# Optimization experiments

Measured on AMD Instinct MI355X. Metric: run time of the kernel, lower is better.

The kernel has to match this reference:

```python
import jax, jax.numpy as jnp
import numpy as np

DIM = 768
NUM_HEADS = 12
HEAD_DIM = DIM // NUM_HEADS
GRID = 32  # H == W
EPS = 1e-6


def setup_inputs() -> dict:
    key = jax.random.key(0)
    ks = jax.random.split(key, 8)
    B, N = 8, GRID * GRID
    x = jax.random.normal(ks[0], (B, N, DIM), dtype=jnp.float32)
    policy = jax.random.randint(ks[1], (B, N, 1), 0, 2).astype(jnp.float32)
    qkv_w = jax.random.normal(ks[2], (3 * DIM, DIM), dtype=jnp.float32) * 0.02
    qkv_b = jax.random.normal(ks[3], (3 * DIM,), dtype=jnp.float32) * 0.02
    proj_w = jax.random.normal(ks[4], (DIM, DIM), dtype=jnp.float32) * 0.02
    proj_b = jax.random.normal(ks[5], (DIM,), dtype=jnp.float32) * 0.02
    rel_pos_h = jax.random.normal(ks[6], (2 * GRID - 1, HEAD_DIM), dtype=jnp.float32) * 0.02
    rel_pos_w = jax.random.normal(ks[7], (2 * GRID - 1, HEAD_DIM), dtype=jnp.float32) * 0.02
    return {"x": x, "policy": policy, "qkv_w": qkv_w, "qkv_b": qkv_b,
            "proj_w": proj_w, "proj_b": proj_b,
            "rel_pos_h": rel_pos_h, "rel_pos_w": rel_pos_w, "H": GRID, "W": GRID}


def _attention(x, policy, qkv_w, qkv_b, proj_w, proj_b, rel_pos_h, rel_pos_w, H, W):
    B, N, C = x.shape
    nh, hd = NUM_HEADS, C // NUM_HEADS
    scale = hd ** (-0.5)
    # qkv projection: [B,N,3C] -> [3, B*nh, N, hd]
    qkv = (x @ qkv_w.T + qkv_b).reshape(B, N, 3, nh, hd)
    qkv = qkv.transpose(2, 0, 3, 1, 4).reshape(3, B * nh, N, hd)
    q, k, v = qkv[0], qkv[1], qkv[2]
    attn = jnp.einsum("bqd,bkd->bqk", q * scale, k)  # [B*nh, N, N]
    # decomposed relative position bias (q_size == k_size == (H, W))
    coords = jnp.arange(H)
    Rh = rel_pos_h[coords[:, None] - coords[None, :] + (H - 1)]  # [H,H,hd]
    coords_w = jnp.arange(W)
    Rw = rel_pos_w[coords_w[:, None] - coords_w[None, :] + (W - 1)]  # [W,W,hd]
    r_q = q.reshape(B * nh, H, W, hd)
    rel_h = jnp.einsum("bhwc,hkc->bhwk", r_q, Rh)  # [B*nh,H,W,H]
    rel_w = jnp.einsum("bhwc,wkc->bhwk", r_q, Rw)  # [B*nh,H,W,W]
    attn = (attn.reshape(B * nh, H, W, H, W)
            + rel_h[:, :, :, :, None]
            + rel_w[:, :, :, None, :]).reshape(B * nh, N, N)
    # policy-masked softmax
    attn = attn.reshape(B, nh, N, N)
    ap = policy.reshape(B, 1, 1, N)
    ap = ap + (1.0 - ap) * jnp.eye(N, dtype=ap.dtype)  # always attend to self
    max_att = jnp.max(attn, axis=-1, keepdims=True)
    e = jnp.exp(attn - max_att).astype(jnp.float32) * ap.astype(jnp.float32)
    attn = ((e + EPS / N) / (jnp.sum(e, axis=-1, keepdims=True) + EPS)).astype(x.dtype)
    out = jnp.einsum("bqk,bkd->bqd", attn.reshape(B * nh, N, N), v)
    out = out.reshape(B, nh, N, hd).transpose(0, 2, 1, 3).reshape(B, N, C)
    return out @ proj_w.T + proj_b


def reference(x, policy, qkv_w, qkv_b, proj_w, proj_b, rel_pos_h, rel_pos_w, H, W):
    return _attention(x, policy, qkv_w, qkv_b, proj_w, proj_b, rel_pos_h, rel_pos_w, H, W)
```

## Files before the change

kernel.cpp:

```cpp
#include <hip/hip_runtime.h>
#include <hip/hip_bf16.h>

#define B_   8
#define N_   1024
#define C_   768
#define NH_  12
#define HD_  64
#define BH_  96
#define EPS_ 1e-6f
#define EPSN_ (1e-6f / 1024.0f)

typedef __bf16 bf16;
typedef __attribute__((ext_vector_type(8))) __bf16  bf16x8;
typedef __attribute__((ext_vector_type(4))) __bf16  bf16x4;
typedef __attribute__((ext_vector_type(4))) float   floatx4;

#define MFMA16(a, b, c) __builtin_amdgcn_mfma_f32_16x16x32_bf16((a), (b), (c), 0, 0, 0)

__global__ __launch_bounds__(256) void f2b_kernel(const float* __restrict__ in,
                                                  bf16* __restrict__ out, int n4) {
  int i = blockIdx.x * 256 + threadIdx.x;
  if (i < n4) {
    float4 v = ((const float4*)in)[i];
    bf16x4 o = {(bf16)v.x, (bf16)v.y, (bf16)v.z, (bf16)v.w};
    ((bf16x4*)out)[i] = o;
  }
}

__global__ __launch_bounds__(256) void rel_kernel(const float* __restrict__ in,
                                                  bf16* __restrict__ out) {
  int i = blockIdx.x * 256 + threadIdx.x;
  int r = i >> 6;
  out[i] = (r < 63) ? (bf16)in[i] : (bf16)0.0f;
}

__global__ __launch_bounds__(256) void gemm_qkv(
    const bf16* __restrict__ X, const bf16* __restrict__ W,
    const float* __restrict__ bias,
    bf16* __restrict__ Qb, bf16* __restrict__ Kb, bf16* __restrict__ Vb) {
  __shared__ bf16 As[128][72];
  __shared__ bf16 Bs[128][72];
  const int tid = threadIdx.x;
  const int wid = tid >> 6, lane = tid & 63, quad = lane >> 4, c16 = lane & 15;
  const int wm = (wid >> 1) * 64, wn = (wid & 1) * 64;
  const int m0 = blockIdx.x * 128, n0 = blockIdx.y * 128;
  floatx4 acc[4][4];
#pragma unroll
  for (int i = 0; i < 4; ++i)
#pragma unroll
    for (int j = 0; j < 4; ++j) acc[i][j] = {0.f, 0.f, 0.f, 0.f};

  for (int k0 = 0; k0 < 768; k0 += 64) {
    __syncthreads();
#pragma unroll
    for (int t = 0; t < 4; ++t) {
      int task = t * 256 + tid;
      int r = task >> 3, c8 = (task & 7) * 8;
      *(bf16x8*)&As[r][c8] = *(const bf16x8*)(X + (size_t)(m0 + r) * 768 + k0 + c8);
      *(bf16x8*)&Bs[r][c8] = *(const bf16x8*)(W + (size_t)(n0 + r) * 768 + k0 + c8);
    }
    __syncthreads();
#pragma unroll
    for (int kw = 0; kw < 2; ++kw) {
      bf16x8 af[4], bfr[4];
#pragma unroll
      for (int i = 0; i < 4; ++i) af[i] = *(bf16x8*)&As[wm + i * 16 + c16][kw * 32 + quad * 8];
#pragma unroll
      for (int j = 0; j < 4; ++j) bfr[j] = *(bf16x8*)&Bs[wn + j * 16 + c16][kw * 32 + quad * 8];
#pragma unroll
      for (int i = 0; i < 4; ++i)
#pragma unroll
        for (int j = 0; j < 4; ++j) acc[i][j] = MFMA16(af[i], bfr[j], acc[i][j]);
    }
  }
#pragma unroll
  for (int jt = 0; jt < 4; ++jt) {
    int j = n0 + wn + jt * 16 + c16;
    float bj = bias[j];
    int t = j / 768, rem = j - t * 768;
    int head = rem >> 6, d = rem & 63;
    bf16* base = (t == 0) ? Qb : (t == 1) ? Kb : Vb;
#pragma unroll
    for (int it = 0; it < 4; ++it)
#pragma unroll
      for (int reg = 0; reg < 4; ++reg) {
        int m = m0 + wm + it * 16 + quad * 4 + reg;
        int bb = m >> 10, n = m & 1023;
        float v = acc[it][jt][reg] + bj;
        size_t idx = (t == 2)
            ? (((size_t)bb * NH_ + head) * HD_ + d) * N_ + n
            : (((size_t)bb * NH_ + head) * N_ + n) * HD_ + d;
        base[idx] = (bf16)v;
      }
  }
}

__global__ __launch_bounds__(256) void vsum_kernel(const bf16* __restrict__ Vb,
                                                   float* __restrict__ Vsum) {
  const int bh = blockIdx.x;
  const int d = threadIdx.x >> 2, part = threadIdx.x & 3;
  const bf16* Vg = Vb + (size_t)bh * (N_ * HD_) + d * N_ + part * 256;
  float s = 0.f;
  for (int i = 0; i < 32; ++i) {
    bf16x8 v = *(const bf16x8*)(Vg + i * 8);
#pragma unroll
    for (int e = 0; e < 8; ++e) s += (float)v[e];
  }
  __shared__ float red[64][4];
  red[d][part] = s;
  __syncthreads();
  if (part == 0) Vsum[bh * 64 + d] = red[d][0] + red[d][1] + red[d][2] + red[d][3];
}

__global__ __launch_bounds__(256) void attn_mfma(
    const bf16* __restrict__ Qb, const bf16* __restrict__ Kb,
    const bf16* __restrict__ Vb, const float* __restrict__ policy,
    const bf16* __restrict__ Rh, const bf16* __restrict__ Rw,
    const float* __restrict__ Vsum, bf16* __restrict__ AO) {
  const int bh = blockIdx.x, qt = blockIdx.y;
  const int b = bh / NH_, head = bh % NH_;
  __shared__ __align__(16) char smem[46592];
  bf16 (*Qs)[72]  = (bf16(*)[72])(smem);
  bf16 (*Ks)[72]  = (bf16(*)[72])(smem + 9216);
  bf16 (*Vt)[72]  = (bf16(*)[72])(smem + 18432);
  float (*RHs)[33] = (float(*)[33])(smem + 27648);
  float (*RWs)[33] = (float(*)[33])(smem + 36096);
  bf16* pol = (bf16*)(smem + 44544);
  const int tid = threadIdx.x;
  const int wid = tid >> 6, lane = tid & 63, quad = lane >> 4, c16 = lane & 15;
  bf16 (*Ptw)[72] = (bf16(*)[72])(smem) + wid * 16;
  const floatx4 zero4 = {0.f, 0.f, 0.f, 0.f};

  const bf16* Qg = Qb + ((size_t)bh * N_ + qt * 64) * HD_;
  const bf16* Kg = Kb + (size_t)bh * (N_ * HD_);
  const bf16* Vg = Vb + (size_t)bh * (N_ * HD_);

#pragma unroll
  for (int t = 0; t < 2; ++t) {
    int task = t * 256 + tid;
    int r = task >> 3, c8 = (task & 7) * 8;
    *(bf16x8*)&Qs[r][c8] = *(const bf16x8*)(Qg + r * 64 + c8);
    *(bf16x8*)&Ks[r][c8] = *(const bf16x8*)(Rh + r * 64 + c8);
  }
  {
    float4 p = ((const float4*)(policy + (size_t)b * N_))[tid];
    bf16x4 pb = {(bf16)p.x, (bf16)p.y, (bf16)p.z, (bf16)p.w};
    *(bf16x4*)&pol[tid * 4] = pb;
  }
  __syncthreads();

  bf16x8 aq0 = *(bf16x8*)&Qs[wid * 16 + c16][quad * 8];
  bf16x8 aq1 = *(bf16x8*)&Qs[wid * 16 + c16][32 + quad * 8];

  {
    floatx4 racc[4];
#pragma unroll
    for (int nt = 0; nt < 4; ++nt) {
      bf16x8 b0 = *(bf16x8*)&Ks[nt * 16 + c16][quad * 8];
      bf16x8 b1 = *(bf16x8*)&Ks[nt * 16 + c16][32 + quad * 8];
      racc[nt] = MFMA16(aq1, b1, MFMA16(aq0, b0, zero4));
    }
#pragma unroll
    for (int nt = 0; nt < 4; ++nt)
#pragma unroll
      for (int reg = 0; reg < 4; ++reg) {
        int rloc = wid * 16 + quad * 4 + reg;
        int hh = 2 * qt + (rloc >> 5);
        int j = nt * 16 + c16;
        int krow = hh + 31 - j;
        if ((unsigned)krow < 32u) RHs[rloc][krow] = racc[nt][reg];
      }
  }
  __syncthreads();
#pragma unroll
  for (int t = 0; t < 2; ++t) {
    int task = t * 256 + tid;
    int r = task >> 3, c8 = (task & 7) * 8;
    *(bf16x8*)&Ks[r][c8] = *(const bf16x8*)(Rw + r * 64 + c8);
  }
  __syncthreads();
  {
    floatx4 racc[4];
#pragma unroll
    for (int nt = 0; nt < 4; ++nt) {
      bf16x8 b0 = *(bf16x8*)&Ks[nt * 16 + c16][quad * 8];
      bf16x8 b1 = *(bf16x8*)&Ks[nt * 16 + c16][32 + quad * 8];
      racc[nt] = MFMA16(aq1, b1, MFMA16(aq0, b0, zero4));
    }
#pragma unroll
    for (int nt = 0; nt < 4; ++nt)
#pragma unroll
      for (int reg = 0; reg < 4; ++reg) {
        int rloc = wid * 16 + quad * 4 + reg;
        int ww = rloc & 31;
        int j = nt * 16 + c16;
        int kcol = ww + 31 - j;
        if ((unsigned)kcol < 32u) RWs[rloc][kcol] = racc[nt][reg];
      }
  }

  float l_part[4] = {0.f, 0.f, 0.f, 0.f};
  floatx4 o_acc[4];
#pragma unroll
  for (int i = 0; i < 4; ++i) o_acc[i] = zero4;
  int nqr[4];
#pragma unroll
  for (int reg = 0; reg < 4; ++reg) nqr[reg] = qt * 64 + wid * 16 + quad * 4 + reg;

  for (int kt = 0; kt < 16; ++kt) {
    __syncthreads();
#pragma unroll
    for (int t = 0; t < 2; ++t) {
      int task = t * 256 + tid;
      int r = task >> 3, c8 = (task & 7) * 8;
      *(bf16x8*)&Ks[r][c8] = *(const bf16x8*)(Kg + (size_t)(kt * 64 + r) * 64 + c8);
      *(bf16x8*)&Vt[r][c8] = *(const bf16x8*)(Vg + (size_t)r * N_ + kt * 64 + c8);
    }
    __syncthreads();

    floatx4 s[4];
#pragma unroll
    for (int nt = 0; nt < 4; ++nt) {
      bf16x8 bk0 = *(bf16x8*)&Ks[nt * 16 + c16][quad * 8];
      bf16x8 bk1 = *(bf16x8*)&Ks[nt * 16 + c16][32 + quad * 8];
      s[nt] = MFMA16(aq1, bk1, MFMA16(aq0, bk0, zero4));
    }
    float pm[4];
#pragma unroll
    for (int nt = 0; nt < 4; ++nt) pm[nt] = (float)pol[kt * 64 + nt * 16 + c16];

#pragma unroll
    for (int reg = 0; reg < 4; ++reg) {
      const int rloc = wid * 16 + quad * 4 + reg;
      const int nq = nqr[reg];
      const float rh0 = RHs[rloc][kt * 2], rh1 = RHs[rloc][kt * 2 + 1];
#pragma unroll
      for (int nt = 0; nt < 4; ++nt) {
        float sv = s[nt][reg] * 0.125f + ((nt < 2) ? rh0 : rh1)
                 + RWs[rloc][(nt & 1) * 16 + c16];
        int kg = kt * 64 + nt * 16 + c16;
        float mask = (kg == nq) ? 1.f : pm[nt];
        float e = __expf(sv) * mask;
        l_part[reg] += e;
        Ptw[quad * 4 + reg][nt * 16 + c16] = (bf16)e;
      }
    }

#pragma unroll
    for (int kw2 = 0; kw2 < 2; ++kw2) {
      bf16x8 ap = *(bf16x8*)&Ptw[c16][kw2 * 32 + quad * 8];
#pragma unroll
      for (int dt = 0; dt < 4; ++dt) {
        bf16x8 bv = *(bf16x8*)&Vt[dt * 16 + c16][kw2 * 32 + quad * 8];
        o_acc[dt] = MFMA16(ap, bv, o_acc[dt]);
      }
    }
  }

  float inv[4];
#pragma unroll
  for (int reg = 0; reg < 4; ++reg) {
    float l = l_part[reg];
#pragma unroll
    for (int d = 1; d < 16; d <<= 1) l += __shfl_xor(l, d, 64);
    inv[reg] = 1.f / (l + EPS_);
  }
#pragma unroll
  for (int dt = 0; dt < 4; ++dt) {
    int d = dt * 16 + c16;
    float vs = Vsum[bh * 64 + d];
#pragma unroll
    for (int reg = 0; reg < 4; ++reg) {
      float o = (o_acc[dt][reg] + EPSN_ * vs) * inv[reg];
      AO[((size_t)b * N_ + nqr[reg]) * C_ + head * HD_ + d] = (bf16)o;
    }
  }
}

__global__ __launch_bounds__(256) void gemm_proj(
    const bf16* __restrict__ A, const bf16* __restrict__ W,
    const float* __restrict__ bias, float* __restrict__ Out) {
  __shared__ bf16 As[128][72];
  __shared__ bf16 Bs[128][72];
  const int tid = threadIdx.x;
  const int wid = tid >> 6, lane = tid & 63, quad = lane >> 4, c16 = lane & 15;
  const int wm = (wid >> 1) * 64, wn = (wid & 1) * 64;
  const int m0 = blockIdx.x * 128, n0 = blockIdx.y * 128;
  floatx4 acc[4][4];
#pragma unroll
  for (int i = 0; i < 4; ++i)
#pragma unroll
    for (int j = 0; j < 4; ++j) acc[i][j] = {0.f, 0.f, 0.f, 0.f};

  for (int k0 = 0; k0 < 768; k0 += 64) {
    __syncthreads();
#pragma unroll
    for (int t = 0; t < 4; ++t) {
      int task = t * 256 + tid;
      int r = task >> 3, c8 = (task & 7) * 8;
      *(bf16x8*)&As[r][c8] = *(const bf16x8*)(A + (size_t)(m0 + r) * 768 + k0 + c8);
      *(bf16x8*)&Bs[r][c8] = *(const bf16x8*)(W + (size_t)(n0 + r) * 768 + k0 + c8);
    }
    __syncthreads();
#pragma unroll
    for (int kw = 0; kw < 2; ++kw) {
      bf16x8 af[4], bfr[4];
#pragma unroll
      for (int i = 0; i < 4; ++i) af[i] = *(bf16x8*)&As[wm + i * 16 + c16][kw * 32 + quad * 8];
#pragma unroll
      for (int j = 0; j < 4; ++j) bfr[j] = *(bf16x8*)&Bs[wn + j * 16 + c16][kw * 32 + quad * 8];
#pragma unroll
      for (int i = 0; i < 4; ++i)
#pragma unroll
        for (int j = 0; j < 4; ++j) acc[i][j] = MFMA16(af[i], bfr[j], acc[i][j]);
    }
  }
#pragma unroll
  for (int jt = 0; jt < 4; ++jt) {
    int j = n0 + wn + jt * 16 + c16;
    float bj = bias[j];
#pragma unroll
    for (int it = 0; it < 4; ++it)
#pragma unroll
      for (int reg = 0; reg < 4; ++reg) {
        int m = m0 + wm + it * 16 + quad * 4 + reg;
        Out[(size_t)m * 768 + j] = acc[it][jt][reg] + bj;
      }
  }
}

extern "C" void kernel_launch(void* const* d_in, const int* in_sizes, int n_in,
                              void* d_out, int out_size, void* d_ws, size_t ws_size,
                              hipStream_t stream) {
  const float* x      = (const float*)d_in[0];
  const float* policy = (const float*)d_in[1];
  const float* qkv_w  = (const float*)d_in[2];
  const float* qkv_b  = (const float*)d_in[3];
  const float* proj_w = (const float*)d_in[4];
  const float* proj_b = (const float*)d_in[5];
  const float* relh   = (const float*)d_in[6];
  const float* relw   = (const float*)d_in[7];

  char* ws = (char*)d_ws;
  bf16* Xbf   = (bf16*)(ws);
  bf16* Wqkv  = (bf16*)(ws + 12582912);
  bf16* Wproj = (bf16*)(ws + 16121856);
  bf16* Rhb   = (bf16*)(ws + 17301504);
  bf16* Rwb   = (bf16*)(ws + 17309696);
  bf16* Qb    = (bf16*)(ws + 17317888);
  bf16* Kb    = (bf16*)(ws + 29900800);
  bf16* Vb    = (bf16*)(ws + 42483712);
  bf16* AOb   = (bf16*)(ws + 55066624);
  float* Vsum = (float*)(ws + 67649536);

  f2b_kernel<<<6144, 256, 0, stream>>>(x, Xbf, 1572864);
  f2b_kernel<<<1728, 256, 0, stream>>>(qkv_w, Wqkv, 442368);
  f2b_kernel<<<576, 256, 0, stream>>>(proj_w, Wproj, 147456);
  rel_kernel<<<16, 256, 0, stream>>>(relh, Rhb);
  rel_kernel<<<16, 256, 0, stream>>>(relw, Rwb);

  gemm_qkv<<<dim3(64, 18), 256, 0, stream>>>(Xbf, Wqkv, qkv_b, Qb, Kb, Vb);
  vsum_kernel<<<BH_, 256, 0, stream>>>(Vb, Vsum);
  attn_mfma<<<dim3(BH_, 16), 256, 0, stream>>>(Qb, Kb, Vb, policy, Rhb, Rwb,
                                               Vsum, AOb);
  gemm_proj<<<dim3(64, 6), 256, 0, stream>>>(AOb, Wproj, proj_b, (float*)d_out);
}
```

Measured before the change: 261.1 us.

## Use direct global-to-LDS loads with XOR swizzle, fold softmax scales, transpose V epilogue

Global-to-shared tile copies in the QKV GEMM, attention and projection kernels now go through global_load_lds 16-byte loads into XOR-swizzled unpadded LDS tiles, which avoids the register round trip and bank conflicts without padding. The attention scale and log2(e) are folded into Q at the QKV epilogue, and the relative-position tables are prescaled by 8, so the softmax can use exp2f without per-element multiplies. The diagonal self-attend mask check only runs on the diagonal key tile. The V-producing GEMM blocks swap MFMA operands so the transposed V store writes contiguous rows. Together these add layout complexity and some bf16 rounding differences from the prescaling.

```diff
diff --git a/kernel.cpp b/kernel.cpp
--- a/kernel.cpp
+++ b/kernel.cpp
@@ -9,6 +9,7 @@
 #define BH_  96
 #define EPS_ 1e-6f
 #define EPSN_ (1e-6f / 1024.0f)
+#define SQ_  0.1803368801111244f
 
 typedef __bf16 bf16;
 typedef __attribute__((ext_vector_type(8))) __bf16  bf16x8;
@@ -16,6 +17,13 @@
 typedef __attribute__((ext_vector_type(4))) float   floatx4;
 
 #define MFMA16(a, b, c) __builtin_amdgcn_mfma_f32_16x16x32_bf16((a), (b), (c), 0, 0, 0)
+
+__device__ __forceinline__ void gld16(const bf16* g, bf16* l) {
+  typedef unsigned int u32;
+  __builtin_amdgcn_global_load_lds(
+      (const __attribute__((address_space(1))) u32*)g,
+      (__attribute__((address_space(3))) u32*)l, 16, 0, 0);
+}
 
 __global__ __launch_bounds__(256) void f2b_kernel(const float* __restrict__ in,
                                                   bf16* __restrict__ out, int n4) {
@@ -31,19 +39,21 @@
                                                   bf16* __restrict__ out) {
   int i = blockIdx.x * 256 + threadIdx.x;
   int r = i >> 6;
-  out[i] = (r < 63) ? (bf16)in[i] : (bf16)0.0f;
+  out[i] = (r < 63) ? (bf16)(in[i] * 8.0f) : (bf16)0.0f;
 }
 
 __global__ __launch_bounds__(256) void gemm_qkv(
     const bf16* __restrict__ X, const bf16* __restrict__ W,
     const float* __restrict__ bias,
     bf16* __restrict__ Qb, bf16* __restrict__ Kb, bf16* __restrict__ Vb) {
-  __shared__ bf16 As[128][72];
-  __shared__ bf16 Bs[128][72];
+  __shared__ __align__(16) bf16 As[128 * 64];
+  __shared__ __align__(16) bf16 Bs[128 * 64];
   const int tid = threadIdx.x;
-  const int wid = tid >> 6, lane = tid & 63, quad = lane >> 4, c16 = lane & 15;
+  const int lane = tid & 63, quad = lane >> 4, c16 = lane & 15;
+  const int wid = tid >> 6;
   const int wm = (wid >> 1) * 64, wn = (wid & 1) * 64;
   const int m0 = blockIdx.x * 128, n0 = blockIdx.y * 128;
+  const bool flip = (blockIdx.y >= 12);
   floatx4 acc[4][4];
 #pragma unroll
   for (int i = 0; i < 4; ++i)
@@ -55,42 +65,87 @@
 #pragma unroll
     for (int t = 0; t < 4; ++t) {
       int task = t * 256 + tid;
-      int r = task >> 3, c8 = (task & 7) * 8;
-      *(bf16x8*)&As[r][c8] = *(const bf16x8*)(X + (size_t)(m0 + r) * 768 + k0 + c8);
-      *(bf16x8*)&Bs[r][c8] = *(const bf16x8*)(W + (size_t)(n0 + r) * 768 + k0 + c8);
-    }
-    __syncthreads();
-#pragma unroll
-    for (int kw = 0; kw < 2; ++kw) {
-      bf16x8 af[4], bfr[4];
-#pragma unroll
-      for (int i = 0; i < 4; ++i) af[i] = *(bf16x8*)&As[wm + i * 16 + c16][kw * 32 + quad * 8];
-#pragma unroll
-      for (int j = 0; j < 4; ++j) bfr[j] = *(bf16x8*)&Bs[wn + j * 16 + c16][kw * 32 + quad * 8];
-#pragma unroll
-      for (int i = 0; i < 4; ++i)
-#pragma unroll
-        for (int j = 0; j < 4; ++j) acc[i][j] = MFMA16(af[i], bfr[j], acc[i][j]);
-    }
-  }
-#pragma unroll
-  for (int jt = 0; jt < 4; ++jt) {
-    int j = n0 + wn + jt * 16 + c16;
-    float bj = bias[j];
-    int t = j / 768, rem = j - t * 768;
-    int head = rem >> 6, d = rem & 63;
-    bf16* base = (t == 0) ? Qb : (t == 1) ? Kb : Vb;
-#pragma unroll
-    for (int it = 0; it < 4; ++it)
+      int r = task >> 3, lg = (task & 7) ^ (r & 7);
+      int wbase = (t * 256 + (tid & 192)) * 8;
+      gld16(X + (size_t)(m0 + r) * 768 + k0 + lg * 8, &As[wbase]);
+      gld16(W + (size_t)(n0 + r) * 768 + k0 + lg * 8, &Bs[wbase]);
+    }
+    __syncthreads();
+    if (!flip) {
+#pragma unroll
+      for (int kw = 0; kw < 2; ++kw) {
+        bf16x8 af[4], bfr[4];
+#pragma unroll
+        for (int i = 0; i < 4; ++i) {
+          int r = wm + i * 16 + c16, pg = (kw * 4 + quad) ^ (c16 & 7);
+          af[i] = *(bf16x8*)&As[r * 64 + pg * 8];
+        }
+#pragma unroll
+        for (int j = 0; j < 4; ++j) {
+          int r = wn + j * 16 + c16, pg = (kw * 4 + quad) ^ (c16 & 7);
+          bfr[j] = *(bf16x8*)&Bs[r * 64 + pg * 8];
+        }
+#pragma unroll
+        for (int i = 0; i < 4; ++i)
+#pragma unroll
+          for (int j = 0; j < 4; ++j) acc[i][j] = MFMA16(af[i], bfr[j], acc[i][j]);
+      }
+    } else {
+#pragma unroll
+      for (int kw = 0; kw < 2; ++kw) {
+        bf16x8 af[4], bfr[4];
+#pragma unroll
+        for (int i = 0; i < 4; ++i) {
+          int r = wm + i * 16 + c16, pg = (kw * 4 + quad) ^ (c16 & 7);
+          af[i] = *(bf16x8*)&As[r * 64 + pg * 8];
+        }
+#pragma unroll
+        for (int j = 0; j < 4; ++j) {
+          int r = wn + j * 16 + c16, pg = (kw * 4 + quad) ^ (c16 & 7);
+          bfr[j] = *(bf16x8*)&Bs[r * 64 + pg * 8];
+        }
+#pragma unroll
+        for (int a = 0; a < 4; ++a)
+#pragma unroll
+          for (int b = 0; b < 4; ++b) acc[a][b] = MFMA16(bfr[a], af[b], acc[a][b]);
+      }
+    }
+  }
+  if (!flip) {
+    const bool isQ = (blockIdx.y < 6);
+    bf16* base = isQ ? Qb : Kb;
+#pragma unroll
+    for (int jt = 0; jt < 4; ++jt) {
+      int j = n0 + wn + jt * 16 + c16;
+      float bj = bias[j];
+      int rem = j - (isQ ? 0 : 768);
+      int head = rem >> 6, d = rem & 63;
+#pragma unroll
+      for (int it = 0; it < 4; ++it)
+#pragma unroll
+        for (int reg = 0; reg < 4; ++reg) {
+          int m = m0 + wm + it * 16 + quad * 4 + reg;
+          int bb = m >> 10, n = m & 1023;
+          float v = acc[it][jt][reg] + bj;
+          if (isQ) v *= SQ_;
+          base[(((size_t)bb * NH_ + head) * N_ + n) * HD_ + d] = (bf16)v;
+        }
+    }
+  } else {
+#pragma unroll
+    for (int a = 0; a < 4; ++a)
 #pragma unroll
       for (int reg = 0; reg < 4; ++reg) {
-        int m = m0 + wm + it * 16 + quad * 4 + reg;
-        int bb = m >> 10, n = m & 1023;
-        float v = acc[it][jt][reg] + bj;
-        size_t idx = (t == 2)
-            ? (((size_t)bb * NH_ + head) * HD_ + d) * N_ + n
-            : (((size_t)bb * NH_ + head) * N_ + n) * HD_ + d;
-        base[idx] = (bf16)v;
+        int j = n0 + wn + a * 16 + quad * 4 + reg;
+        float bj = bias[j];
+        int rem = j - 1536;
+        int head = rem >> 6, d = rem & 63;
+#pragma unroll
+        for (int b = 0; b < 4; ++b) {
+          int m = m0 + wm + b * 16 + c16;
+          int bb = m >> 10, n = m & 1023;
+          Vb[(((size_t)bb * NH_ + head) * HD_ + d) * N_ + n] = (bf16)(acc[a][b][reg] + bj);
+        }
       }
   }
 }
@@ -119,16 +174,16 @@
     const float* __restrict__ Vsum, bf16* __restrict__ AO) {
   const int bh = blockIdx.x, qt = blockIdx.y;
   const int b = bh / NH_, head = bh % NH_;
-  __shared__ __align__(16) char smem[46592];
-  bf16 (*Qs)[72]  = (bf16(*)[72])(smem);
-  bf16 (*Ks)[72]  = (bf16(*)[72])(smem + 9216);
-  bf16 (*Vt)[72]  = (bf16(*)[72])(smem + 18432);
-  float (*RHs)[33] = (float(*)[33])(smem + 27648);
-  float (*RWs)[33] = (float(*)[33])(smem + 36096);
-  bf16* pol = (bf16*)(smem + 44544);
+  __shared__ __align__(16) bf16 Qs[4096];
+  __shared__ __align__(16) bf16 Ks[4096];
+  __shared__ __align__(16) bf16 Vt[4096];
+  __shared__ float RHs[64][33];
+  __shared__ float RWs[64][33];
+  __shared__ bf16 pol[1024];
   const int tid = threadIdx.x;
   const int wid = tid >> 6, lane = tid & 63, quad = lane >> 4, c16 = lane & 15;
-  bf16 (*Ptw)[72] = (bf16(*)[72])(smem) + wid * 16;
+  const int sw = c16 & 7;
+  bf16* Ptw = Qs + wid * 1024;
   const floatx4 zero4 = {0.f, 0.f, 0.f, 0.f};
 
   const bf16* Qg = Qb + ((size_t)bh * N_ + qt * 64) * HD_;
@@ -138,9 +193,10 @@
 #pragma unroll
   for (int t = 0; t < 2; ++t) {
     int task = t * 256 + tid;
-    int r = task >> 3, c8 = (task & 7) * 8;
-    *(bf16x8*)&Qs[r][c8] = *(const bf16x8*)(Qg + r * 64 + c8);
-    *(bf16x8*)&Ks[r][c8] = *(const bf16x8*)(Rh + r * 64 + c8);
+    int r = task >> 3, lg = (task & 7) ^ (r & 7);
+    int wbase = (t * 256 + (tid & 192)) * 8;
+    gld16(Qg + r * 64 + lg * 8, &Qs[wbase]);
+    gld16(Rh + r * 64 + lg * 8, &Ks[wbase]);
   }
   {
     float4 p = ((const float4*)(policy + (size_t)b * N_))[tid];
@@ -149,15 +205,16 @@
   }
   __syncthreads();
 
-  bf16x8 aq0 = *(bf16x8*)&Qs[wid * 16 + c16][quad * 8];
-  bf16x8 aq1 = *(bf16x8*)&Qs[wid * 16 + c16][32 + quad * 8];
+  bf16x8 aq0 = *(bf16x8*)&Qs[(wid * 16 + c16) * 64 + (quad ^ sw) * 8];
+  bf16x8 aq1 = *(bf16x8*)&Qs[(wid * 16 + c16) * 64 + ((4 + quad) ^ sw) * 8];
 
   {
     floatx4 racc[4];
 #pragma unroll
     for (int nt = 0; nt < 4; ++nt) {
-      bf16x8 b0 = *(bf16x8*)&Ks[nt * 16 + c16][quad * 8];
-      bf16x8 b1 = *(bf16x8*)&Ks[nt * 16 + c16][32 + quad * 8];
+      int r = nt * 16 + c16;
+      bf16x8 b0 = *(bf16x8*)&Ks[r * 64 + (quad ^ sw) * 8];
+      bf16x8 b1 = *(bf16x8*)&Ks[r * 64 + ((4 + quad) ^ sw) * 8];
       racc[nt] = MFMA16(aq1, b1, MFMA16(aq0, b0, zero4));
     }
 #pragma unroll
@@ -166,8 +223,7 @@
       for (int reg = 0; reg < 4; ++reg) {
         int rloc = wid * 16 + quad * 4 + reg;
         int hh = 2 * qt + (rloc >> 5);
-        int j = nt * 16 + c16;
-        int krow = hh + 31 - j;
+        int krow = hh + 31 - (nt * 16 + c16);
         if ((unsigned)krow < 32u) RHs[rloc][krow] = racc[nt][reg];
       }
   }
@@ -175,16 +231,17 @@
 #pragma unroll
   for (int t = 0; t < 2; ++t) {
     int task = t * 256 + tid;
-    int r = task >> 3, c8 = (task & 7) * 8;
-    *(bf16x8*)&Ks[r][c8] = *(const bf16x8*)(Rw + r * 64 + c8);
+    int r = task >> 3, lg = (task & 7) ^ (r & 7);
+    gld16(Rw + r * 64 + lg * 8, &Ks[(t * 256 + (tid & 192)) * 8]);
   }
   __syncthreads();
   {
     floatx4 racc[4];
 #pragma unroll
     for (int nt = 0; nt < 4; ++nt) {
-      bf16x8 b0 = *(bf16x8*)&Ks[nt * 16 + c16][quad * 8];
-      bf16x8 b1 = *(bf16x8*)&Ks[nt * 16 + c16][32 + quad * 8];
+      int r = nt * 16 + c16;
+      bf16x8 b0 = *(bf16x8*)&Ks[r * 64 + (quad ^ sw) * 8];
+      bf16x8 b1 = *(bf16x8*)&Ks[r * 64 + ((4 + quad) ^ sw) * 8];
       racc[nt] = MFMA16(aq1, b1, MFMA16(aq0, b0, zero4));
     }
 #pragma unroll
@@ -192,9 +249,7 @@
 #pragma unroll
       for (int reg = 0; reg < 4; ++reg) {
         int rloc = wid * 16 + quad * 4 + reg;
-        int ww = rloc & 31;
-        int j = nt * 16 + c16;
-        int kcol = ww + 31 - j;
+        int kcol = (rloc & 31) + 31 - (nt * 16 + c16);
         if ((unsigned)kcol < 32u) RWs[rloc][kcol] = racc[nt][reg];
       }
   }
@@ -212,17 +267,19 @@
 #pragma unroll
     for (int t = 0; t < 2; ++t) {
       int task = t * 256 + tid;
-      int r = task >> 3, c8 = (task & 7) * 8;
-      *(bf16x8*)&Ks[r][c8] = *(const bf16x8*)(Kg + (size_t)(kt * 64 + r) * 64 + c8);
-      *(bf16x8*)&Vt[r][c8] = *(const bf16x8*)(Vg + (size_t)r * N_ + kt * 64 + c8);
+      int r = task >> 3, lg = (task & 7) ^ (r & 7);
+      int wbase = (t * 256 + (tid & 192)) * 8;
+      gld16(Kg + (size_t)(kt * 64 + r) * 64 + lg * 8, &Ks[wbase]);
+      gld16(Vg + (size_t)r * N_ + kt * 64 + lg * 8, &Vt[wbase]);
     }
     __syncthreads();
 
     floatx4 s[4];
 #pragma unroll
     for (int nt = 0; nt < 4; ++nt) {
-      bf16x8 bk0 = *(bf16x8*)&Ks[nt * 16 + c16][quad * 8];
-      bf16x8 bk1 = *(bf16x8*)&Ks[nt * 16 + c16][32 + quad * 8];
+      int r = nt * 16 + c16;
+      bf16x8 bk0 = *(bf16x8*)&Ks[r * 64 + (quad ^ sw) * 8];
+      bf16x8 bk1 = *(bf16x8*)&Ks[r * 64 + ((4 + quad) ^ sw) * 8];
       s[nt] = MFMA16(aq1, bk1, MFMA16(aq0, bk0, zero4));
     }
     float pm[4];
@@ -232,26 +289,41 @@
 #pragma unroll
     for (int reg = 0; reg < 4; ++reg) {
       const int rloc = wid * 16 + quad * 4 + reg;
-      const int nq = nqr[reg];
+      const int prow = quad * 4 + reg;
       const float rh0 = RHs[rloc][kt * 2], rh1 = RHs[rloc][kt * 2 + 1];
-#pragma unroll
-      for (int nt = 0; nt < 4; ++nt) {
-        float sv = s[nt][reg] * 0.125f + ((nt < 2) ? rh0 : rh1)
-                 + RWs[rloc][(nt & 1) * 16 + c16];
-        int kg = kt * 64 + nt * 16 + c16;
-        float mask = (kg == nq) ? 1.f : pm[nt];
-        float e = __expf(sv) * mask;
-        l_part[reg] += e;
-        Ptw[quad * 4 + reg][nt * 16 + c16] = (bf16)e;
+      if (kt != qt) {
+#pragma unroll
+        for (int nt = 0; nt < 4; ++nt) {
+          float sv = s[nt][reg] + ((nt < 2) ? rh0 : rh1)
+                   + RWs[rloc][(nt & 1) * 16 + c16];
+          float e = exp2f(sv) * pm[nt];
+          l_part[reg] += e;
+          int pg = ((nt * 2 + (c16 >> 3)) ^ (prow & 7));
+          Ptw[prow * 64 + pg * 8 + (c16 & 7)] = (bf16)e;
+        }
+      } else {
+        const int nq = nqr[reg];
+#pragma unroll
+        for (int nt = 0; nt < 4; ++nt) {
+          float sv = s[nt][reg] + ((nt < 2) ? rh0 : rh1)
+                   + RWs[rloc][(nt & 1) * 16 + c16];
+          int kg = kt * 64 + nt * 16 + c16;
+          float mask = (kg == nq) ? 1.f : pm[nt];
+          float e = exp2f(sv) * mask;
+          l_part[reg] += e;
+          int pg = ((nt * 2 + (c16 >> 3)) ^ (prow & 7));
+          Ptw[prow * 64 + pg * 8 + (c16 & 7)] = (bf16)e;
+        }
       }
     }
 
 #pragma unroll
     for (int kw2 = 0; kw2 < 2; ++kw2) {
-      bf16x8 ap = *(bf16x8*)&Ptw[c16][kw2 * 32 + quad * 8];
+      bf16x8 ap = *(bf16x8*)&Ptw[c16 * 64 + ((kw2 * 4 + quad) ^ sw) * 8];
 #pragma unroll
       for (int dt = 0; dt < 4; ++dt) {
-        bf16x8 bv = *(bf16x8*)&Vt[dt * 16 + c16][kw2 * 32 + quad * 8];
+        int r = dt * 16 + c16;
+        bf16x8 bv = *(bf16x8*)&Vt[r * 64 + ((kw2 * 4 + quad) ^ sw) * 8];
         o_acc[dt] = MFMA16(ap, bv, o_acc[dt]);
       }
     }
@@ -280,10 +352,11 @@
 __global__ __launch_bounds__(256) void gemm_proj(
     const bf16* __restrict__ A, const bf16* __restrict__ W,
     const float* __restrict__ bias, float* __restrict__ Out) {
-  __shared__ bf16 As[128][72];
-  __shared__ bf16 Bs[128][72];
+  __shared__ __align__(16) bf16 As[128 * 64];
+  __shared__ __align__(16) bf16 Bs[128 * 64];
   const int tid = threadIdx.x;
-  const int wid = tid >> 6, lane = tid & 63, quad = lane >> 4, c16 = lane & 15;
+  const int lane = tid & 63, quad = lane >> 4, c16 = lane & 15;
+  const int wid = tid >> 6;
   const int wm = (wid >> 1) * 64, wn = (wid & 1) * 64;
   const int m0 = blockIdx.x * 128, n0 = blockIdx.y * 128;
   floatx4 acc[4][4];
@@ -297,18 +370,25 @@
 #pragma unroll
     for (int t = 0; t < 4; ++t) {
       int task = t * 256 + tid;
-      int r = task >> 3, c8 = (task & 7) * 8;
-      *(bf16x8*)&As[r][c8] = *(const bf16x8*)(A + (size_t)(m0 + r) * 768 + k0 + c8);
-      *(bf16x8*)&Bs[r][c8] = *(const bf16x8*)(W + (size_t)(n0 + r) * 768 + k0 + c8);
+      int r = task >> 3, lg = (task & 7) ^ (r & 7);
+      int wbase = (t * 256 + (tid & 192)) * 8;
+      gld16(A + (size_t)(m0 + r) * 768 + k0 + lg * 8, &As[wbase]);
+      gld16(W + (size_t)(n0 + r) * 768 + k0 + lg * 8, &Bs[wbase]);
     }
     __syncthreads();
 #pragma unroll
     for (int kw = 0; kw < 2; ++kw) {
       bf16x8 af[4], bfr[4];
 #pragma unroll
-      for (int i = 0; i < 4; ++i) af[i] = *(bf16x8*)&As[wm + i * 16 + c16][kw * 32 + quad * 8];
-#pragma unroll
-      for (int j = 0; j < 4; ++j) bfr[j] = *(bf16x8*)&Bs[wn + j * 16 + c16][kw * 32 + quad * 8];
+      for (int i = 0; i < 4; ++i) {
+        int r = wm + i * 16 + c16, pg = (kw * 4 + quad) ^ (c16 & 7);
+        af[i] = *(bf16x8*)&As[r * 64 + pg * 8];
+      }
+#pragma unroll
+      for (int j = 0; j < 4; ++j) {
+        int r = wn + j * 16 + c16, pg = (kw * 4 + quad) ^ (c16 & 7);
+        bfr[j] = *(bf16x8*)&Bs[r * 64 + pg * 8];
+      }
 #pragma unroll
       for (int i = 0; i < 4; ++i)
 #pragma unroll
```

Result: faster. 253.3 us (-3.0%).
